# Kernel tuning notes

Measured on AMD Instinct MI355X. Metric: run time of the kernel, lower is better.

Reference implementation:

```python
import jax, jax.numpy as jnp
import numpy as np

NQ = 4          # wires=4 in the PennyLane device
NLAYERS = 4     # num_layers default
AX = 'abcd'     # one einsum letter per qubit axis


def _apply_1q(state, U, w):
    """Apply a 2x2 (or batched (B,2,2)) unitary to qubit axis w of state (B,2,2,2,2)."""
    sub = AX[w]
    out = AX[:w] + 'x' + AX[w + 1:]
    if U.ndim == 3:
        return jnp.einsum(f'zx{sub},z{AX}->z{out}', U, state)
    return jnp.einsum(f'x{sub},z{AX}->z{out}', U, state)


def _apply_cnot(state, c, t):
    """CNOT with control qubit c, target qubit t (static wire indices)."""
    s0 = jax.lax.index_in_dim(state, 0, axis=c + 1, keepdims=True)
    s1 = jax.lax.index_in_dim(state, 1, axis=c + 1, keepdims=True)
    s1 = jnp.flip(s1, axis=t + 1)  # flip target amplitudes where control = 1
    return jnp.concatenate([s0, s1], axis=c + 1)


def _rot(phi, theta, omega):
    """PennyLane Rot gate: RZ(omega) @ RY(theta) @ RZ(phi), as a 2x2 complex matrix."""
    c = jnp.cos(theta * 0.5)
    s = jnp.sin(theta * 0.5)
    em = jnp.exp(-0.5j * (phi + omega))   # e^{-i(phi+omega)/2}, complex64 (weak 1j)
    ed = jnp.exp(0.5j * (phi - omega))    # e^{+i(phi-omega)/2}
    return jnp.stack([
        jnp.stack([em * c, -ed * s]),
        jnp.stack([jnp.conj(ed) * s, jnp.conj(em) * c]),
    ])


def _forward(inputs, q_weights):
    B = inputs.shape[0]
    # |0000> statevector, batched
    state = jnp.zeros((B, 2 ** NQ), jnp.complex64).at[:, 0].set(1.0)
    state = state.reshape((B,) + (2,) * NQ)

    # AngleEmbedding with rotation='Y': RY(x_w) on each wire w (per-sample angles)
    half = inputs * 0.5
    c, s = jnp.cos(half), jnp.sin(half)
    for w in range(NQ):
        U = jnp.stack([jnp.stack([c[:, w], -s[:, w]], axis=-1),
                       jnp.stack([s[:, w], c[:, w]], axis=-1)], axis=-2)
        state = _apply_1q(state, U.astype(jnp.complex64), w)

    # One StronglyEntanglingLayers block per layer of q_weights:
    # per-qubit Rot gates followed by a ring of CNOTs (range r=1 for single-layer calls)
    n_layers = q_weights.shape[0]
    for l in range(n_layers):
        for w in range(NQ):
            state = _apply_1q(state, _rot(q_weights[l, w, 0],
                                          q_weights[l, w, 1],
                                          q_weights[l, w, 2]), w)
        for w in range(NQ):
            state = _apply_cnot(state, w, (w + 1) % NQ)

    # <Z_i> for each wire: marginal prob of bit i, contracted with diag(+1,-1)
    probs = state.real ** 2 + state.imag ** 2  # (B,2,2,2,2)
    z = jnp.array([1.0, -1.0], jnp.float32)
    expvals = []
    for w in range(NQ):
        reduce_axes = tuple(i + 1 for i in range(NQ) if i != w)
        p = probs.sum(axis=reduce_axes)  # (B,2)
        expvals.append(p @ z)
    return jnp.stack(expvals, axis=-1)  # (B,4)


def setup_inputs() -> dict:
    key = jax.random.key(0)
    k1, k2 = jax.random.split(key)
    B = 1048576
    inputs = jax.random.normal(k1, (B, NQ), dtype=jnp.float32)
    # glorot_uniform for shape (4,4,3): limit = sqrt(6/(fan_in+fan_out))
    limit = np.sqrt(6.0 / (NQ * 3 + NQ * 3)).astype(np.float32)
    q_weights = jax.random.uniform(k2, (NLAYERS, NQ, 3), dtype=jnp.float32,
                                   minval=-limit, maxval=limit)
    return {"inputs": inputs, "q_weights": q_weights}


def reference(inputs, q_weights):
    return _forward(inputs, q_weights)
```

## Files before the change

### kernel.cpp

```cpp
#include <hip/hip_runtime.h>
#include <math.h>


__global__ __launch_bounds__(256) void build_C(const float* __restrict__ qw,
                                               float* __restrict__ Cg) {
    __shared__ float g[16][8];
    __shared__ float Ar[2][16][16];
    __shared__ float Ai[2][16][16];
    __shared__ float ReE[4][16][16];
    int t = threadIdx.x;
    int b   = t >> 4;
    int col = t & 15;

    if (t < 16) {
        float phi = qw[t * 3 + 0], theta = qw[t * 3 + 1], omega = qw[t * 3 + 2];
        float st, ct, sha, cha, shd, chd;
        __sincosf(0.5f * theta, &st, &ct);
        __sincosf(0.5f * (phi + omega), &sha, &cha);
        __sincosf(0.5f * (phi - omega), &shd, &chd);
        g[t][0] =  cha * ct; g[t][1] = -sha * ct;
        g[t][2] = -chd * st; g[t][3] = -shd * st;
        g[t][4] =  chd * st; g[t][5] = -shd * st;
        g[t][6] =  cha * ct; g[t][7] =  sha * ct;
    }
    Ar[0][b][col] = (b == col) ? 1.f : 0.f;
    Ai[0][b][col] = 0.f;
    __syncthreads();

    int perm = b;
#pragma unroll
    for (int w = 3; w >= 0; --w) {
        int cm = 8 >> w, tm = 8 >> ((w + 1) & 3);
        perm = (perm & cm) ? (perm ^ tm) : perm;
    }

    int p = 0;
    for (int l = 0; l < 4; ++l) {
#pragma unroll
        for (int w = 0; w < 4; ++w) {
            int gi = l * 4 + w;
            int m = 8 >> w;
            int lo = b & ~m, hi = b | m;
            bool isHi = (b & m) != 0;
            float cAr = isHi ? g[gi][4] : g[gi][0];
            float cAi = isHi ? g[gi][5] : g[gi][1];
            float cBr = isHi ? g[gi][6] : g[gi][2];
            float cBi = isHi ? g[gi][7] : g[gi][3];
            float alor = Ar[p][lo][col], aloi = Ai[p][lo][col];
            float ahir = Ar[p][hi][col], ahii = Ai[p][hi][col];
            float nr = cAr * alor - cAi * aloi + cBr * ahir - cBi * ahii;
            float ni = cAr * aloi + cAi * alor + cBr * ahii + cBi * ahir;
            Ar[1 - p][b][col] = nr;
            Ai[1 - p][b][col] = ni;
            p = 1 - p;
            __syncthreads();
        }
        float nr = Ar[p][perm][col], ni = Ai[p][perm][col];
        Ar[1 - p][b][col] = nr;
        Ai[1 - p][b][col] = ni;
        p = 1 - p;
        __syncthreads();
    }

    for (int idx = t; idx < 1024; idx += 256) {
        int w = idx >> 8, i = (idx >> 4) & 15, j = idx & 15;
        float acc = 0.f;
#pragma unroll
        for (int bb = 0; bb < 16; ++bb) {
            float z = ((bb >> (3 - w)) & 1) ? -1.f : 1.f;
            acc += z * (Ar[p][bb][i] * Ar[p][bb][j] + Ai[p][bb][i] * Ai[p][bb][j]);
        }
        ReE[w][i][j] = acc;
    }
    __syncthreads();

    for (int idx = t; idx < 324; idx += 256) {
        int w = idx & 3, tt = idx >> 2;
        int t01 = tt / 9, t23 = tt % 9;
        int d0 = t01 / 3, d1 = t01 % 3, d2 = t23 / 3, d3 = t23 % 3;
        int xmask = ((d0 == 1) << 3) | ((d1 == 1) << 2) | ((d2 == 1) << 1) | (d3 == 1);
        int zmask = ((d0 == 2) << 3) | ((d1 == 2) << 2) | ((d2 == 2) << 1) | (d3 == 2);
        float acc = 0.f;
#pragma unroll
        for (int i = 0; i < 16; ++i) {
            float sgn = (__popc(i & zmask) & 1) ? -1.f : 1.f;
            acc += sgn * ReE[w][i][i ^ xmask];
        }
        Cg[idx] = acc * 0.0625f;
    }
}

__global__ __launch_bounds__(256) void qlayer_main(
        const float4* __restrict__ x, const float* __restrict__ Cg,
        float4* __restrict__ out, int B) {
    __shared__ __align__(16) float C[324];
    for (int k = threadIdx.x; k < 324; k += 256) C[k] = Cg[k];
    __syncthreads();

    int half = B >> 1;
    int i = blockIdx.x * 256 + threadIdx.x;
    if (i >= half) {
        if (i == half && (B & 1)) {
            float4 xv = x[B - 1];
            float s0, c0, s1, c1, s2, c2, s3, c3;
            __sincosf(xv.x, &s0, &c0); __sincosf(xv.y, &s1, &c1);
            __sincosf(xv.z, &s2, &c2); __sincosf(xv.w, &s3, &c3);
            float m0[3] = {1.f, s0, c0}, m1[3] = {1.f, s1, c1};
            float m2[3] = {1.f, s2, c2}, m3[3] = {1.f, s3, c3};
            float e0 = 0.f, e1 = 0.f, e2 = 0.f, e3 = 0.f;
            for (int t01 = 0; t01 < 9; ++t01)
                for (int t23 = 0; t23 < 9; ++t23) {
                    float mv = m0[t01 / 3] * m1[t01 % 3] * m2[t23 / 3] * m3[t23 % 3];
                    const float4 c4 = *(const float4*)&C[(t01 * 9 + t23) * 4];
                    e0 = fmaf(c4.x, mv, e0); e1 = fmaf(c4.y, mv, e1);
                    e2 = fmaf(c4.z, mv, e2); e3 = fmaf(c4.w, mv, e3);
                }
            out[B - 1] = make_float4(e0, e1, e2, e3);
        }
        return;
    }

    float4 xa = x[i];
    float4 xb = x[i + half];
    float as0, ac0, as1, ac1, as2, ac2, as3, ac3;
    float bs0, bc0, bs1, bc1, bs2, bc2, bs3, bc3;
    __sincosf(xa.x, &as0, &ac0); __sincosf(xa.y, &as1, &ac1);
    __sincosf(xa.z, &as2, &ac2); __sincosf(xa.w, &as3, &ac3);
    __sincosf(xb.x, &bs0, &bc0); __sincosf(xb.y, &bs1, &bc1);
    __sincosf(xb.z, &bs2, &bc2); __sincosf(xb.w, &bs3, &bc3);

    float am0[3] = {1.f, as0, ac0}, am1[3] = {1.f, as1, ac1};
    float am2[3] = {1.f, as2, ac2}, am3[3] = {1.f, as3, ac3};
    float bm0[3] = {1.f, bs0, bc0}, bm1[3] = {1.f, bs1, bc1};
    float bm2[3] = {1.f, bs2, bc2}, bm3[3] = {1.f, bs3, bc3};
    float aM01[9], aM23[9], bM01[9], bM23[9];
#pragma unroll
    for (int a = 0; a < 3; ++a)
#pragma unroll
        for (int c = 0; c < 3; ++c) {
            aM01[a * 3 + c] = am0[a] * am1[c];
            aM23[a * 3 + c] = am2[a] * am3[c];
            bM01[a * 3 + c] = bm0[a] * bm1[c];
            bM23[a * 3 + c] = bm2[a] * bm3[c];
        }

    float ae0 = 0.f, ae1 = 0.f, ae2 = 0.f, ae3 = 0.f;
    float be0 = 0.f, be1 = 0.f, be2 = 0.f, be3 = 0.f;
#pragma unroll
    for (int t01 = 0; t01 < 9; ++t01) {
        float ah0 = 0.f, ah1 = 0.f, ah2 = 0.f, ah3 = 0.f;
        float bh0 = 0.f, bh1 = 0.f, bh2 = 0.f, bh3 = 0.f;
#pragma unroll
        for (int t23 = 0; t23 < 9; ++t23) {
            const float4 c4 = *(const float4*)&C[(t01 * 9 + t23) * 4];
            float av = aM23[t23], bv = bM23[t23];
            ah0 = fmaf(c4.x, av, ah0); bh0 = fmaf(c4.x, bv, bh0);
            ah1 = fmaf(c4.y, av, ah1); bh1 = fmaf(c4.y, bv, bh1);
            ah2 = fmaf(c4.z, av, ah2); bh2 = fmaf(c4.z, bv, bh2);
            ah3 = fmaf(c4.w, av, ah3); bh3 = fmaf(c4.w, bv, bh3);
        }
        float au = aM01[t01], bu = bM01[t01];
        ae0 = fmaf(au, ah0, ae0); be0 = fmaf(bu, bh0, be0);
        ae1 = fmaf(au, ah1, ae1); be1 = fmaf(bu, bh1, be1);
        ae2 = fmaf(au, ah2, ae2); be2 = fmaf(bu, bh2, be2);
        ae3 = fmaf(au, ah3, ae3); be3 = fmaf(bu, bh3, be3);
    }
    out[i]        = make_float4(ae0, ae1, ae2, ae3);
    out[i + half] = make_float4(be0, be1, be2, be3);
}

extern "C" void kernel_launch(void* const* d_in, const int* in_sizes, int n_in,
                              void* d_out, int out_size, void* d_ws, size_t ws_size,
                              hipStream_t stream) {
    const float4* x  = (const float4*)d_in[0];
    const float*  qw = (const float*)d_in[1];
    float* Cg = (float*)d_ws;
    float4* out = (float4*)d_out;
    int B = in_sizes[0] / 4;

    hipLaunchKernelGGL(build_C, dim3(1), dim3(256), 0, stream, qw, Cg);

    int half = B >> 1;
    int blocks = (half + 255) / 256;
    if (blocks < 1) blocks = 1;
    hipLaunchKernelGGL(qlayer_main, dim3(blocks), dim3(256), 0, stream,
                       x, Cg, out, B);
}
```

Measured before the change: 81.10 us.

## Fuse coefficient build into main kernel and process four samples per thread

Removes the separate single-block build_C launch. Every block now recomputes the 324-entry coefficient table in shared memory, and the input loads and sincos calls are issued first so their latency overlaps with that build. Each thread now handles four samples instead of two, which spreads each shared-memory coefficient read over more FMAs. The cost is redundant per-block table construction, with many __syncthreads, across about 1024 blocks, plus higher register pressure.

```diff
diff --git a/kernel.cpp b/kernel.cpp
--- a/kernel.cpp
+++ b/kernel.cpp
@@ -2,15 +2,41 @@
 #include <math.h>
 
 
-__global__ __launch_bounds__(256) void build_C(const float* __restrict__ qw,
-                                               float* __restrict__ Cg) {
+__global__ __launch_bounds__(256) void qlayer_fused(
+        const float4* __restrict__ x, const float* __restrict__ qw,
+        float4* __restrict__ out, int B) {
     __shared__ float g[16][8];
     __shared__ float Ar[2][16][16];
     __shared__ float Ai[2][16][16];
     __shared__ float ReE[4][16][16];
-    int t = threadIdx.x;
-    int b   = t >> 4;
-    int col = t & 15;
+    __shared__ __align__(16) float C[324];
+
+    const int t = threadIdx.x;
+    const int b = t >> 4, col = t & 15;
+    const int Q = (B + 3) >> 2;
+    const int i0 = blockIdx.x * 256 + t;
+    const bool act = (i0 < Q);
+
+    float4 xs[4];
+#pragma unroll
+    for (int k = 0; k < 4; ++k) {
+        int ik = i0 + k * Q;
+        xs[k] = (act && ik < B) ? x[ik] : make_float4(0.f, 0.f, 0.f, 0.f);
+    }
+    float s0[4], c0[4], s1[4], c1[4], M23[4][9];
+#pragma unroll
+    for (int k = 0; k < 4; ++k) {
+        float s2v, c2v, s3v, c3v;
+        __sincosf(xs[k].x, &s0[k], &c0[k]);
+        __sincosf(xs[k].y, &s1[k], &c1[k]);
+        __sincosf(xs[k].z, &s2v, &c2v);
+        __sincosf(xs[k].w, &s3v, &c3v);
+        float m2[3] = {1.f, s2v, c2v}, m3[3] = {1.f, s3v, c3v};
+#pragma unroll
+        for (int a = 0; a < 3; ++a)
+#pragma unroll
+            for (int d = 0; d < 3; ++d) M23[k][a * 3 + d] = m2[a] * m3[d];
+    }
 
     if (t < 16) {
         float phi = qw[t * 3 + 0], theta = qw[t * 3 + 1], omega = qw[t * 3 + 2];
@@ -86,87 +112,56 @@
             float sgn = (__popc(i & zmask) & 1) ? -1.f : 1.f;
             acc += sgn * ReE[w][i][i ^ xmask];
         }
-        Cg[idx] = acc * 0.0625f;
+        C[idx] = acc * 0.0625f;
     }
-}
-
-__global__ __launch_bounds__(256) void qlayer_main(
-        const float4* __restrict__ x, const float* __restrict__ Cg,
-        float4* __restrict__ out, int B) {
-    __shared__ __align__(16) float C[324];
-    for (int k = threadIdx.x; k < 324; k += 256) C[k] = Cg[k];
     __syncthreads();
 
-    int half = B >> 1;
-    int i = blockIdx.x * 256 + threadIdx.x;
-    if (i >= half) {
-        if (i == half && (B & 1)) {
-            float4 xv = x[B - 1];
-            float s0, c0, s1, c1, s2, c2, s3, c3;
-            __sincosf(xv.x, &s0, &c0); __sincosf(xv.y, &s1, &c1);
-            __sincosf(xv.z, &s2, &c2); __sincosf(xv.w, &s3, &c3);
-            float m0[3] = {1.f, s0, c0}, m1[3] = {1.f, s1, c1};
-            float m2[3] = {1.f, s2, c2}, m3[3] = {1.f, s3, c3};
-            float e0 = 0.f, e1 = 0.f, e2 = 0.f, e3 = 0.f;
-            for (int t01 = 0; t01 < 9; ++t01)
-                for (int t23 = 0; t23 < 9; ++t23) {
-                    float mv = m0[t01 / 3] * m1[t01 % 3] * m2[t23 / 3] * m3[t23 % 3];
-                    const float4 c4 = *(const float4*)&C[(t01 * 9 + t23) * 4];
-                    e0 = fmaf(c4.x, mv, e0); e1 = fmaf(c4.y, mv, e1);
-                    e2 = fmaf(c4.z, mv, e2); e3 = fmaf(c4.w, mv, e3);
+    float e[4][4];
+#pragma unroll
+    for (int k = 0; k < 4; ++k)
+#pragma unroll
+        for (int w = 0; w < 4; ++w) e[k][w] = 0.f;
+
+#pragma unroll
+    for (int a = 0; a < 3; ++a) {
+#pragma unroll
+        for (int d = 0; d < 3; ++d) {
+            const int t01 = a * 3 + d;
+            float h[4][4];
+#pragma unroll
+            for (int k = 0; k < 4; ++k)
+#pragma unroll
+                for (int w = 0; w < 4; ++w) h[k][w] = 0.f;
+#pragma unroll
+            for (int t23 = 0; t23 < 9; ++t23) {
+                const float4 c4 = *(const float4*)&C[(t01 * 9 + t23) * 4];
+#pragma unroll
+                for (int k = 0; k < 4; ++k) {
+                    float mv = M23[k][t23];
+                    h[k][0] = fmaf(c4.x, mv, h[k][0]);
+                    h[k][1] = fmaf(c4.y, mv, h[k][1]);
+                    h[k][2] = fmaf(c4.z, mv, h[k][2]);
+                    h[k][3] = fmaf(c4.w, mv, h[k][3]);
                 }
-            out[B - 1] = make_float4(e0, e1, e2, e3);
+            }
+#pragma unroll
+            for (int k = 0; k < 4; ++k) {
+                float m0a = (a == 0) ? 1.f : ((a == 1) ? s0[k] : c0[k]);
+                float m1d = (d == 0) ? 1.f : ((d == 1) ? s1[k] : c1[k]);
+                float mu = m0a * m1d;
+                e[k][0] = fmaf(mu, h[k][0], e[k][0]);
+                e[k][1] = fmaf(mu, h[k][1], e[k][1]);
+                e[k][2] = fmaf(mu, h[k][2], e[k][2]);
+                e[k][3] = fmaf(mu, h[k][3], e[k][3]);
+            }
         }
-        return;
     }
-
-    float4 xa = x[i];
-    float4 xb = x[i + half];
-    float as0, ac0, as1, ac1, as2, ac2, as3, ac3;
-    float bs0, bc0, bs1, bc1, bs2, bc2, bs3, bc3;
-    __sincosf(xa.x, &as0, &ac0); __sincosf(xa.y, &as1, &ac1);
-    __sincosf(xa.z, &as2, &ac2); __sincosf(xa.w, &as3, &ac3);
-    __sincosf(xb.x, &bs0, &bc0); __sincosf(xb.y, &bs1, &bc1);
-    __sincosf(xb.z, &bs2, &bc2); __sincosf(xb.w, &bs3, &bc3);
-
-    float am0[3] = {1.f, as0, ac0}, am1[3] = {1.f, as1, ac1};
-    float am2[3] = {1.f, as2, ac2}, am3[3] = {1.f, as3, ac3};
-    float bm0[3] = {1.f, bs0, bc0}, bm1[3] = {1.f, bs1, bc1};
-    float bm2[3] = {1.f, bs2, bc2}, bm3[3] = {1.f, bs3, bc3};
-    float aM01[9], aM23[9], bM01[9], bM23[9];
 #pragma unroll
-    for (int a = 0; a < 3; ++a)
-#pragma unroll
-        for (int c = 0; c < 3; ++c) {
-            aM01[a * 3 + c] = am0[a] * am1[c];
-            aM23[a * 3 + c] = am2[a] * am3[c];
-            bM01[a * 3 + c] = bm0[a] * bm1[c];
-            bM23[a * 3 + c] = bm2[a] * bm3[c];
-        }
-
-    float ae0 = 0.f, ae1 = 0.f, ae2 = 0.f, ae3 = 0.f;
-    float be0 = 0.f, be1 = 0.f, be2 = 0.f, be3 = 0.f;
-#pragma unroll
-    for (int t01 = 0; t01 < 9; ++t01) {
-        float ah0 = 0.f, ah1 = 0.f, ah2 = 0.f, ah3 = 0.f;
-        float bh0 = 0.f, bh1 = 0.f, bh2 = 0.f, bh3 = 0.f;
-#pragma unroll
-        for (int t23 = 0; t23 < 9; ++t23) {
-            const float4 c4 = *(const float4*)&C[(t01 * 9 + t23) * 4];
-            float av = aM23[t23], bv = bM23[t23];
-            ah0 = fmaf(c4.x, av, ah0); bh0 = fmaf(c4.x, bv, bh0);
-            ah1 = fmaf(c4.y, av, ah1); bh1 = fmaf(c4.y, bv, bh1);
-            ah2 = fmaf(c4.z, av, ah2); bh2 = fmaf(c4.z, bv, bh2);
-            ah3 = fmaf(c4.w, av, ah3); bh3 = fmaf(c4.w, bv, bh3);
-        }
-        float au = aM01[t01], bu = bM01[t01];
-        ae0 = fmaf(au, ah0, ae0); be0 = fmaf(bu, bh0, be0);
-        ae1 = fmaf(au, ah1, ae1); be1 = fmaf(bu, bh1, be1);
-        ae2 = fmaf(au, ah2, ae2); be2 = fmaf(bu, bh2, be2);
-        ae3 = fmaf(au, ah3, ae3); be3 = fmaf(bu, bh3, be3);
+    for (int k = 0; k < 4; ++k) {
+        int ik = i0 + k * Q;
+        if (act && ik < B)
+            out[ik] = make_float4(e[k][0], e[k][1], e[k][2], e[k][3]);
     }
-    out[i]        = make_float4(ae0, ae1, ae2, ae3);
-    out[i + half] = make_float4(be0, be1, be2, be3);
 }
 
 extern "C" void kernel_launch(void* const* d_in, const int* in_sizes, int n_in,
@@ -174,15 +169,12 @@
                               hipStream_t stream) {
     const float4* x  = (const float4*)d_in[0];
     const float*  qw = (const float*)d_in[1];
-    float* Cg = (float*)d_ws;
     float4* out = (float4*)d_out;
     int B = in_sizes[0] / 4;
 
-    hipLaunchKernelGGL(build_C, dim3(1), dim3(256), 0, stream, qw, Cg);
-
-    int half = B >> 1;
-    int blocks = (half + 255) / 256;
+    int Q = (B + 3) >> 2;
+    int blocks = (Q + 255) / 256;
     if (blocks < 1) blocks = 1;
-    hipLaunchKernelGGL(qlayer_main, dim3(blocks), dim3(256), 0, stream,
-                       x, Cg, out, B);
+    hipLaunchKernelGGL(qlayer_fused, dim3(blocks), dim3(256), 0, stream,
+                       x, qw, out, B);
 }
```

Result: slower. 101.0 us (+24.6%).
